# Optimization experiments

Hardware: AMD Instinct MI355X
Metric: run time of the kernel (lower is better)

## Reference

```python
import jax, jax.numpy as jnp
import numpy as np

MAX_LEVEL = 50

def _ln(x, g, b, eps=1e-5):
    m = jnp.mean(x, axis=-1, keepdims=True)
    v = jnp.mean((x - m) ** 2, axis=-1, keepdims=True)
    return (x - m) * jax.lax.rsqrt(v + eps) * g + b

def _mlp2(x, w1, b1, w2, b2):
    return jax.nn.relu(x @ w1 + b1) @ w2 + b2

def _forward(tokens, ln_g, ln_b, pw1, pb1, pw2, pb2, emb,
             sw1, sb1, sw2, sb2, ew1, eb1, ew2, eb2,
             spw1, spb1, spw2, spb2, lw1, lb1, lw2, lb2,
             fw, fb, fg, fbeta, aW, ab, ag, abt,
             dw1, db1, dw2, db2, levels, ph, pw):
    N = tokens.shape[0]
    f32 = tokens.dtype
    # token_norm + token_projection (Dropout is identity in eval)
    x = _ln(tokens, ln_g, ln_b)
    h = jax.nn.gelu(x @ pw1 + pb1, approximate=False) @ pw2 + pb2  # [N, D]
    idx = jnp.clip(levels[:, 0], 0, MAX_LEVEL)  # [N]
    h = h + emb[idx]
    # feature enhancement branch
    var = jnp.var(tokens, axis=-1, ddof=1, keepdims=True)            # torch.var unbiased
    mean = jnp.mean(tokens, axis=-1, keepdims=True)
    edge = jnp.mean(jnp.abs(jnp.diff(tokens, axis=-1)), axis=-1, keepdims=True)
    stats_feat = _mlp2(jnp.concatenate([var, mean], -1), sw1, sb1, sw2, sb2)
    spatial = jnp.broadcast_to(jnp.array([[ph, pw]], dtype=f32), (N, 2))
    spatial_feat = _mlp2(spatial, spw1, spb1, spw2, spb2)
    edge_feat = _mlp2(edge, ew1, eb1, ew2, eb2)
    lvl = jnp.broadcast_to(levels[0, 0].astype(f32)[None, None], (N, 1))
    level_feat = _mlp2(lvl, lw1, lb1, lw2, lb2)
    enh = jnp.concatenate([stats_feat, edge_feat, spatial_feat, level_feat], -1)  # [N, D]
    enh = jax.nn.gelu(_ln(enh @ fw + fb, fg, fbeta), approximate=False)
    h = h + 0.3 * enh
    # per-token scale adapter: MoE-style gather + tiny per-token GEMM + per-expert LN + GELU
    y = jnp.einsum('nd,ndf->nf', h, aW[idx]) + ab[idx]
    y = jax.nn.gelu(_ln(y, ag[idx], abt[idx]), approximate=False)
    # dynamic weighting gate
    w = jax.nn.sigmoid(_mlp2(y, dw1, db1, dw2, db2))  # [N, 1]
    return y * (0.8 + 0.4 * w)


def setup_inputs() -> dict:
    key = jax.random.key(0)
    ks = iter(jax.random.split(key, 64))
    def rn(shape, s=0.02):
        return jax.random.normal(next(ks), shape, dtype=jnp.float32) * s
    IN, D, D2, D4, DH, E, N = 768, 256, 512, 64, 128, 51, 4096
    return {
        'tokens': jax.random.normal(next(ks), (N, IN), dtype=jnp.float32),
        'ln_g': jnp.ones((IN,)), 'ln_b': jnp.zeros((IN,)),
        'pw1': rn((IN, D2)), 'pb1': jnp.zeros((D2,)),
        'pw2': rn((D2, D)), 'pb2': jnp.zeros((D,)),
        'emb': rn((E, D), 1.0),
        'sw1': rn((2, D4)), 'sb1': jnp.zeros((D4,)), 'sw2': rn((D4, D4)), 'sb2': jnp.zeros((D4,)),
        'ew1': rn((1, D4)), 'eb1': jnp.zeros((D4,)), 'ew2': rn((D4, D4)), 'eb2': jnp.zeros((D4,)),
        'spw1': rn((2, D4)), 'spb1': jnp.zeros((D4,)), 'spw2': rn((D4, D4)), 'spb2': jnp.zeros((D4,)),
        'lw1': rn((1, D4)), 'lb1': jnp.zeros((D4,)), 'lw2': rn((D4, D4)), 'lb2': jnp.zeros((D4,)),
        'fw': rn((D, D)), 'fb': jnp.zeros((D,)), 'fg': jnp.ones((D,)), 'fbeta': jnp.zeros((D,)),
        'aW': rn((E, D, D)), 'ab': jnp.zeros((E, D)), 'ag': jnp.ones((E, D)), 'abt': jnp.zeros((E, D)),
        'dw1': rn((D, DH)), 'db1': jnp.zeros((DH,)), 'dw2': rn((DH, 1)), 'db2': jnp.zeros((1,)),
        'levels': jax.random.randint(next(ks), (N, 2), 0, E),
        'ph': 4, 'pw': 4,
    }


def reference(tokens, ln_g, ln_b, pw1, pb1, pw2, pb2, emb,
              sw1, sb1, sw2, sb2, ew1, eb1, ew2, eb2,
              spw1, spb1, spw2, spb2, lw1, lb1, lw2, lb2,
              fw, fb, fg, fbeta, aW, ab, ag, abt,
              dw1, db1, dw2, db2, levels, ph, pw):
    return _forward(tokens, ln_g, ln_b, pw1, pb1, pw2, pb2, emb,
                    sw1, sb1, sw2, sb2, ew1, eb1, ew2, eb2,
                    spw1, spb1, spw2, spb2, lw1, lb1, lw2, lb2,
                    fw, fb, fg, fbeta, aW, ab, ag, abt,
                    dw1, db1, dw2, db2, levels, ph, pw)
```

## Files before the change

### kernel.cpp

```cpp
#include <hip/hip_runtime.h>
#include <math.h>

#define NTOK 4096
#define IND 768
#define DD 256
#define DD2 512
#define DHH 128
#define NEXP 51
#define TM 32
#define NTILE_MAX 179
#define NWCONV 968

typedef __attribute__((ext_vector_type(4))) float f32x4;
typedef __attribute__((ext_vector_type(8))) short short8;

__device__ __forceinline__ float gelu_f(float x) {
    return 0.5f * x * (1.0f + erff(x * 0.70710678118654752440f));
}
__device__ __forceinline__ ushort f2bf(float x) {
    unsigned u = __float_as_uint(x);
    return (ushort)((u + 0x7fffu + ((u >> 16) & 1u)) >> 16);
}
__device__ __forceinline__ void gl_lds16(const ushort* g, ushort* l) {
    __builtin_amdgcn_global_load_lds(
        (const __attribute__((address_space(1))) unsigned int*)g,
        (__attribute__((address_space(3))) unsigned int*)l, 16, 0, 0);
}

__global__ __launch_bounds__(256) void k_pre(
    const float* __restrict__ pw1, const float* __restrict__ pw2,
    const float* __restrict__ fw, const float* __restrict__ dw1,
    const float* __restrict__ aW,
    ushort* __restrict__ pw1T, ushort* __restrict__ pw2T, ushort* __restrict__ fwT,
    ushort* __restrict__ dw1T, ushort* __restrict__ aWT,
    const float* __restrict__ tokens,
    const float* __restrict__ ln_g, const float* __restrict__ ln_b,
    const float* __restrict__ sw1, const float* __restrict__ sb1,
    const float* __restrict__ sw2, const float* __restrict__ sb2,
    const float* __restrict__ ew1, const float* __restrict__ eb1,
    const float* __restrict__ ew2, const float* __restrict__ eb2,
    ushort* __restrict__ x_ln, ushort* __restrict__ enh,
    const int* __restrict__ levels,
    const float* __restrict__ spw1, const float* __restrict__ spb1,
    const float* __restrict__ spw2, const float* __restrict__ spb2,
    const float* __restrict__ lw1, const float* __restrict__ lb1,
    const float* __restrict__ lw2, const float* __restrict__ lb2,
    const int* __restrict__ ph, const int* __restrict__ pw,
    const float* __restrict__ fb,
    int* __restrict__ sorted, int* __restrict__ tpos, int* __restrict__ tcnt,
    int* __restrict__ texp, int* __restrict__ meta, float* __restrict__ ctail) {
    __shared__ float T[64][65];
    __shared__ int cnt[NEXP], cur[NEXP], offS[NEXP + 1], tileoff[NEXP + 1];
    __shared__ int expS[NTOK];
    __shared__ float hsS[64], hlS[64], cf[128];
    int t = threadIdx.x;

    if (blockIdx.x == 0) {
        if (t < NEXP) cnt[t] = 0;
        if (t < 64) {
            float p0 = (float)ph[0], p1 = (float)pw[0];
            float lvl = (float)levels[0];
            hsS[t] = fmaxf(0.f, p0 * spw1[t] + p1 * spw1[64 + t] + spb1[t]);
            hlS[t] = fmaxf(0.f, lvl * lw1[t] + lb1[t]);
        }
        __syncthreads();
        int myidx[16];
        #pragma unroll
        for (int i = 0; i < 16; ++i) {
            int n = t + i * 256;
            int id = min(max(levels[n * 2], 0), NEXP - 1);
            myidx[i] = id;
            atomicAdd(&cnt[id], 1);
        }
        if (t < 64) {
            float v = spb2[t];
            for (int j = 0; j < 64; ++j) v += hsS[j] * spw2[j * 64 + t];
            cf[t] = v;
        } else if (t < 128) {
            int k = t - 64;
            float v = lb2[k];
            for (int j = 0; j < 64; ++j) v += hlS[j] * lw2[j * 64 + k];
            cf[64 + k] = v;
        }
        __syncthreads();
        if (t == 0) {
            int a = 0, ta = 0;
            for (int e = 0; e < NEXP; ++e) {
                offS[e] = a; cur[e] = a; tileoff[e] = ta;
                ta += (cnt[e] + TM - 1) / TM;
                a += cnt[e];
            }
            offS[NEXP] = a; tileoff[NEXP] = ta;
            meta[0] = ta;
        }
        __syncthreads();
        #pragma unroll
        for (int i = 0; i < 16; ++i) {
            int n = t + i * 256;
            int p = atomicAdd(&cur[myidx[i]], 1);
            sorted[p] = n;
            expS[p] = myidx[i];
        }
        {
            float v = fb[t];
            for (int j = 0; j < 128; ++j) v += cf[j] * fw[(size_t)(128 + j) * DD + t];
            ctail[t] = v;
        }
        __syncthreads();
        #pragma unroll
        for (int i = 0; i < 16; ++i) {
            int p = t + i * 256;
            int e = expS[p];
            int rel = p - offS[e];
            if ((rel & (TM - 1)) == 0) {
                int ti = tileoff[e] + (rel / TM);
                tpos[ti] = p;
                tcnt[ti] = min(TM, offS[e + 1] - p);
                texp[ti] = e;
            }
        }
        return;
    }
    if (blockIdx.x < 1 + NWCONV) {
        int b = blockIdx.x - 1;
        const float* src; ushort* dst; int R, C;
        if (b < 96)       { src = pw1; dst = pw1T; R = IND; C = DD2; }
        else if (b < 128) { b -= 96;  src = pw2; dst = pw2T; R = DD2; C = DD; }
        else if (b < 144) { b -= 128; src = fw;  dst = fwT;  R = DD;  C = DD; }
        else if (b < 152) { b -= 144; src = dw1; dst = dw1T; R = DD;  C = DHH; }
        else { b -= 152; int e = b >> 4; b &= 15;
               src = aW + (size_t)e * DD * DD; dst = aWT + (size_t)e * DD * DD;
               R = DD; C = DD; }
        int tpc = C >> 6;
        int tr = b / tpc, tc = b - tr * tpc;
        int lr = t >> 6, lc = t & 63;
        #pragma unroll
        for (int i = 0; i < 16; ++i) {
            int r = i * 4 + lr;
            T[r][lc] = src[(size_t)(tr * 64 + r) * C + tc * 64 + lc];
        }
        __syncthreads();
        #pragma unroll
        for (int i = 0; i < 16; ++i) {
            int r = i * 4 + lr;
            dst[(size_t)(tc * 64 + r) * R + tr * 64 + lc] = f2bf(T[lc][r]);
        }
        return;
    }
    {
        int w = t >> 6, lane = t & 63;
        int n = (blockIdx.x - 1 - NWCONV) * 4 + w;
        const float* x = tokens + (size_t)n * IND;
        float v[12];
        {
            float4 va = *(const float4*)(x + lane * 12);
            float4 vb = *(const float4*)(x + lane * 12 + 4);
            float4 vc = *(const float4*)(x + lane * 12 + 8);
            v[0]=va.x; v[1]=va.y; v[2]=va.z; v[3]=va.w;
            v[4]=vb.x; v[5]=vb.y; v[6]=vb.z; v[7]=vb.w;
            v[8]=vc.x; v[9]=vc.y; v[10]=vc.z; v[11]=vc.w;
        }
        float s = 0.f, s2 = 0.f, es = 0.f;
        #pragma unroll
        for (int j = 0; j < 12; ++j) { s += v[j]; s2 += v[j] * v[j]; }
        float prev = __shfl_up(v[11], 1);
        if (lane > 0) es += fabsf(v[0] - prev);
        #pragma unroll
        for (int j = 1; j < 12; ++j) es += fabsf(v[j] - v[j - 1]);
        #pragma unroll
        for (int o = 1; o < 64; o <<= 1) {
            s  += __shfl_xor(s, o);
            s2 += __shfl_xor(s2, o);
            es += __shfl_xor(es, o);
        }
        float mean = s * (1.f / 768.f);
        float var_u = (s2 - 768.f * mean * mean) * (1.f / 767.f);
        float rstd = rsqrtf(s2 * (1.f / 768.f) - mean * mean + 1e-5f);
        float edge = es * (1.f / 767.f);
        ushort xl[12];
        #pragma unroll
        for (int j = 0; j < 12; ++j) {
            int e = lane * 12 + j;
            xl[j] = f2bf((v[j] - mean) * rstd * ln_g[e] + ln_b[e]);
        }
        ushort* xd = x_ln + (size_t)n * IND + lane * 12;
        *(ushort4*)(xd)     = *(ushort4*)&xl[0];
        *(ushort4*)(xd + 4) = *(ushort4*)&xl[4];
        *(ushort4*)(xd + 8) = *(ushort4*)&xl[8];
        float hs_ = fmaxf(0.f, var_u * sw1[lane] + mean * sw1[64 + lane] + sb1[lane]);
        float he_ = fmaxf(0.f, edge * ew1[lane] + eb1[lane]);
        float acc_s = sb2[lane], acc_e = eb2[lane];
        #pragma unroll 8
        for (int j = 0; j < 64; ++j) {
            float hj = __shfl(hs_, j);
            float ej = __shfl(he_, j);
            acc_s += hj * sw2[j * 64 + lane];
            acc_e += ej * ew2[j * 64 + lane];
        }
        ushort* er = enh + (size_t)n * DHH;
        er[lane] = f2bf(acc_s);
        er[64 + lane] = f2bf(acc_e);
    }
}

__global__ __launch_bounds__(512) void k_gemm1(
    const ushort* __restrict__ A, const ushort* __restrict__ BT,
    const float* __restrict__ bias, ushort* __restrict__ Cb) {
    const int N = DD2, K = IND;
    __shared__ ushort Al[128][64];
    __shared__ ushort Bl[64][64];
    int tid = threadIdx.x;
    int w = tid >> 6, lane = tid & 63;
    int g = lane >> 4, mr = lane & 15;
    int mq = w >> 1, nq = w & 1;
    int bm = blockIdx.y * 128, bn = blockIdx.x * 64;
    int r8 = lane >> 3, c = lane & 7, cg = c ^ r8;
    f32x4 acc[2][2];
    #pragma unroll
    for (int im = 0; im < 2; ++im)
        #pragma unroll
        for (int in = 0; in < 2; ++in) acc[im][in] = (f32x4){0.f, 0.f, 0.f, 0.f};
    for (int k0 = 0; k0 < K; k0 += 64) {
        #pragma unroll
        for (int i = 0; i < 2; ++i) {
            int r = 16 * w + 8 * i + r8;
            gl_lds16(A + (size_t)(bm + r) * K + k0 + cg * 8, &Al[16 * w + 8 * i][0]);
        }
        {
            int r = 8 * w + r8;
            gl_lds16(BT + (size_t)(bn + r) * K + k0 + cg * 8, &Bl[8 * w][0]);
        }
        asm volatile("s_waitcnt vmcnt(0)" ::: "memory");
        __syncthreads();
        #pragma unroll
        for (int kk = 0; kk < 64; kk += 32) {
            int jc = (kk >> 3) + g;
            int sw = ((jc ^ (mr & 7)) << 4);
            #pragma unroll
            for (int im = 0; im < 2; ++im) {
                short8 av = *(const short8*)((const char*)&Al[0][0] + (32 * mq + 16 * im + mr) * 128 + sw);
                #pragma unroll
                for (int in = 0; in < 2; ++in) {
                    short8 bv = *(const short8*)((const char*)&Bl[0][0] + (32 * nq + 16 * in + mr) * 128 + sw);
                    acc[im][in] = __builtin_amdgcn_mfma_f32_16x16x32_bf16(av, bv, acc[im][in], 0, 0, 0);
                }
            }
        }
        __syncthreads();
    }
    #pragma unroll
    for (int im = 0; im < 2; ++im) {
        #pragma unroll
        for (int in = 0; in < 2; ++in) {
            int col = bn + 32 * nq + 16 * in + mr;
            float bv = bias[col];
            #pragma unroll
            for (int r = 0; r < 4; ++r) {
                int row = bm + 32 * mq + 16 * im + 4 * g + r;
                Cb[(size_t)row * N + col] = f2bf(gelu_f(acc[im][in][r] + bv));
            }
        }
    }
}

__global__ __launch_bounds__(512) void k_adapterF(
    const ushort* __restrict__ h1, const ushort* __restrict__ enh,
    const ushort* __restrict__ pw2T, const float* __restrict__ pb2,
    const float* __restrict__ emb,
    const ushort* __restrict__ fwT, const float* __restrict__ ctail,
    const float* __restrict__ fg, const float* __restrict__ fbeta,
    const ushort* __restrict__ aWT, const float* __restrict__ ab,
    const float* __restrict__ ag, const float* __restrict__ abt,
    const ushort* __restrict__ dw1T, const float* __restrict__ db1,
    const float* __restrict__ dw2, const float* __restrict__ db2,
    const int* __restrict__ sorted, const int* __restrict__ tpos,
    const int* __restrict__ tcnt, const int* __restrict__ texp,
    const int* __restrict__ meta, float* __restrict__ out) {
    __shared__ __align__(16) char smA[33280];
    __shared__ __align__(16) char smB[33280];
    __shared__ __align__(16) ushort EnhS[TM][128];
    __shared__ int tokS[TM];
    __shared__ float redS[4][TM][2];
    __shared__ float gateS[TM];
    __shared__ float pg[4][TM];
    ushort* H1p = (ushort*)smA;
    ushort* Alf = (ushort*)smA;
    ushort* Dlp = (ushort*)(smA + 16896);
    ushort* Blp = (ushort*)smB;
    float* yf32 = (float*)smB;

    int b = blockIdx.x;
    if (b >= meta[0]) return;
    int tid = threadIdx.x, w = tid >> 6, lane = tid & 63;
    int g = lane >> 4, mr = lane & 15;
    int r8 = lane >> 3, c = lane & 7, cg = c ^ r8;
    int mt = w & 1, cb = 64 * (w >> 1);
    int e = texp[b], base = tpos[b], nv = tcnt[b];
    if (tid < TM) tokS[tid] = sorted[base + min(tid, nv - 1)];
    __syncthreads();

    #pragma unroll
    for (int i = 0; i < 4; ++i) {
        int r = 4 * w + i;
        int tok = tokS[r];
        gl_lds16(h1 + (size_t)tok * DD2 + ((lane ^ (r & 7)) << 3), H1p + r * DD2);
    }
    {
        int row = 4 * w + (lane >> 4);
        int tok = tokS[row];
        int ch = lane & 15;
        gl_lds16(enh + (size_t)tok * DHH + ((ch ^ (row & 7)) << 3), &EnhS[4 * w][0]);
    }
    asm volatile("s_waitcnt vmcnt(0)" ::: "memory");
    __syncthreads();

    f32x4 hacc[4];
    #pragma unroll
    for (int q = 0; q < 4; ++q) hacc[q] = (f32x4){0.f, 0.f, 0.f, 0.f};
    for (int k0 = 0; k0 < DD2; k0 += 64) {
        #pragma unroll
        for (int i = 0; i < 4; ++i) {
            int r = 32 * w + 8 * i + r8;
            gl_lds16(pw2T + (size_t)r * DD2 + k0 + cg * 8, Blp + (32 * w + 8 * i) * 64);
        }
        asm volatile("s_waitcnt vmcnt(0)" ::: "memory");
        __syncthreads();
        #pragma unroll
        for (int kk = 0; kk < 64; kk += 32) {
            int jc = ((k0 + kk) >> 3) + g;
            short8 av = *(const short8*)((const char*)H1p + (16 * mt + mr) * 1024 + ((jc ^ (mr & 7)) << 4));
            int swb = (((kk >> 3) + g) ^ (mr & 7)) << 4;
            #pragma unroll
            for (int q = 0; q < 4; ++q) {
                short8 bv = *(const short8*)((const char*)Blp + (cb + 16 * q + mr) * 128 + swb);
                hacc[q] = __builtin_amdgcn_mfma_f32_16x16x32_bf16(av, bv, hacc[q], 0, 0, 0);
            }
        }
        __syncthreads();
    }
    f32x4 eacc[4];
    #pragma unroll
    for (int q = 0; q < 4; ++q) eacc[q] = (f32x4){0.f, 0.f, 0.f, 0.f};
    for (int k0 = 0; k0 < DHH; k0 += 64) {
        #pragma unroll
        for (int i = 0; i < 4; ++i) {
            int r = 32 * w + 8 * i + r8;
            gl_lds16(fwT + (size_t)r * DD + k0 + cg * 8, Blp + (32 * w + 8 * i) * 64);
        }
        asm volatile("s_waitcnt vmcnt(0)" ::: "memory");
        __syncthreads();
        #pragma unroll
        for (int kk = 0; kk < 64; kk += 32) {
            int jc = ((k0 + kk) >> 3) + g;
            short8 av = *(const short8*)((const char*)&EnhS[0][0] + (16 * mt + mr) * 256 + ((jc ^ (mr & 7)) << 4));
            int swb = (((kk >> 3) + g) ^ (mr & 7)) << 4;
            #pragma unroll
            for (int q = 0; q < 4; ++q) {
                short8 bv = *(const short8*)((const char*)Blp + (cb + 16 * q + mr) * 128 + swb);
                eacc[q] = __builtin_amdgcn_mfma_f32_16x16x32_bf16(av, bv, eacc[q], 0, 0, 0);
            }
        }
        __syncthreads();
    }
    #pragma unroll
    for (int q = 0; q < 4; ++q) {
        int col = cb + 16 * q + mr;
        float hb = pb2[col] + emb[(size_t)e * DD + col];
        float cb2 = ctail[col];
        #pragma unroll
        for (int r4 = 0; r4 < 4; ++r4) {
            hacc[q][r4] += hb;
            eacc[q][r4] += cb2;
        }
    }
    {
        float s[4], s2[4];
        #pragma unroll
        for (int r4 = 0; r4 < 4; ++r4) {
            s[r4] = eacc[0][r4] + eacc[1][r4] + eacc[2][r4] + eacc[3][r4];
            s2[r4] = eacc[0][r4]*eacc[0][r4] + eacc[1][r4]*eacc[1][r4]
                   + eacc[2][r4]*eacc[2][r4] + eacc[3][r4]*eacc[3][r4];
        }
        #pragma unroll
        for (int o = 1; o < 16; o <<= 1) {
            #pragma unroll
            for (int r4 = 0; r4 < 4; ++r4) {
                s[r4]  += __shfl_xor(s[r4], o);
                s2[r4] += __shfl_xor(s2[r4], o);
            }
        }
        if (mr == 0) {
            #pragma unroll
            for (int r4 = 0; r4 < 4; ++r4) {
                int row = 16 * mt + 4 * g + r4;
                redS[w >> 1][row][0] = s[r4];
                redS[w >> 1][row][1] = s2[r4];
            }
        }
    }
    __syncthreads();
    #pragma unroll
    for (int r4 = 0; r4 < 4; ++r4) {
        int row = 16 * mt + 4 * g + r4;
        float S  = redS[0][row][0] + redS[1][row][0] + redS[2][row][0] + redS[3][row][0];
        float S2 = redS[0][row][1] + redS[1][row][1] + redS[2][row][1] + redS[3][row][1];
        float m = S * (1.f / 256.f);
        float rs = rsqrtf(S2 * (1.f / 256.f) - m * m + 1e-5f);
        #pragma unroll
        for (int q = 0; q < 4; ++q) {
            int col = cb + 16 * q + mr;
            float enhv = gelu_f((eacc[q][r4] - m) * rs * fg[col] + fbeta[col]);
            Alf[row * 264 + col] = f2bf(hacc[q][r4] + 0.3f * enhv);
        }
    }
    __syncthreads();
    const ushort* We = aWT + (size_t)e * DD * DD;
    f32x4 yacc[4];
    #pragma unroll
    for (int q = 0; q < 4; ++q) yacc[q] = (f32x4){0.f, 0.f, 0.f, 0.f};
    for (int k0 = 0; k0 < DD; k0 += 64) {
        #pragma unroll
        for (int i = 0; i < 4; ++i) {
            int r = 32 * w + 8 * i + r8;
            gl_lds16(We + (size_t)r * DD + k0 + cg * 8, Blp + (32 * w + 8 * i) * 64);
        }
        asm volatile("s_waitcnt vmcnt(0)" ::: "memory");
        __syncthreads();
        #pragma unroll
        for (int kk = 0; kk < 64; kk += 32) {
            short8 av = *(const short8*)&Alf[(16 * mt + mr) * 264 + k0 + kk + g * 8];
            int swb = (((kk >> 3) + g) ^ (mr & 7)) << 4;
            #pragma unroll
            for (int q = 0; q < 4; ++q) {
                short8 bv = *(const short8*)((const char*)Blp + (cb + 16 * q + mr) * 128 + swb);
                yacc[q] = __builtin_amdgcn_mfma_f32_16x16x32_bf16(av, bv, yacc[q], 0, 0, 0);
            }
        }
        __syncthreads();
    }
    #pragma unroll
    for (int q = 0; q < 4; ++q) {
        int col = cb + 16 * q + mr;
        float abv = ab[(size_t)e * DD + col];
        #pragma unroll
        for (int r4 = 0; r4 < 4; ++r4) {
            int row = 16 * mt + 4 * g + r4;
            yf32[row * 260 + col] = yacc[q][r4] + abv;
        }
    }
    __syncthreads();
    #pragma unroll
    for (int i = 0; i < 4; ++i) {
        int r = 4 * w + i;
        float4 v = *(const float4*)&yf32[r * 260 + lane * 4];
        float s = v.x + v.y + v.z + v.w;
        float s2 = v.x * v.x + v.y * v.y + v.z * v.z + v.w * v.w;
        #pragma unroll
        for (int o = 1; o < 64; o <<= 1) { s += __shfl_xor(s, o); s2 += __shfl_xor(s2, o); }
        float m = s * (1.f / 256.f);
        float rs = rsqrtf(s2 * (1.f / 256.f) - m * m + 1e-5f);
        float4 gg = *(const float4*)(ag + (size_t)e * DD + lane * 4);
        float4 bb = *(const float4*)(abt + (size_t)e * DD + lane * 4);
        float4 y;
        y.x = gelu_f((v.x - m) * rs * gg.x + bb.x);
        y.y = gelu_f((v.y - m) * rs * gg.y + bb.y);
        y.z = gelu_f((v.z - m) * rs * gg.z + bb.z);
        y.w = gelu_f((v.w - m) * rs * gg.w + bb.w);
        *(float4*)&yf32[r * 260 + lane * 4] = y;
        ushort4 o4 = {f2bf(y.x), f2bf(y.y), f2bf(y.z), f2bf(y.w)};
        *(ushort4*)&Alf[r * 264 + lane * 4] = o4;
    }
    __syncthreads();
    f32x4 acc2[2];
    acc2[0] = (f32x4){0.f, 0.f, 0.f, 0.f};
    acc2[1] = (f32x4){0.f, 0.f, 0.f, 0.f};
    for (int k0 = 0; k0 < DD; k0 += 64) {
        #pragma unroll
        for (int i = 0; i < 2; ++i) {
            int r = 16 * w + 8 * i + r8;
            gl_lds16(dw1T + (size_t)r * DD + k0 + cg * 8, Dlp + (16 * w + 8 * i) * 64);
        }
        asm volatile("s_waitcnt vmcnt(0)" ::: "memory");
        __syncthreads();
        #pragma unroll
        for (int kk = 0; kk < 64; kk += 32) {
            short8 av = *(const short8*)&Alf[(16 * mt + mr) * 264 + k0 + kk + g * 8];
            int swb = (((kk >> 3) + g) ^ (mr & 7)) << 4;
            #pragma unroll
            for (int q = 0; q < 2; ++q) {
                short8 bv = *(const short8*)((const char*)Dlp + (32 * (w >> 1) + 16 * q + mr) * 128 + swb);
                acc2[q] = __builtin_amdgcn_mfma_f32_16x16x32_bf16(av, bv, acc2[q], 0, 0, 0);
            }
        }
        __syncthreads();
    }
    float pv[4] = {0.f, 0.f, 0.f, 0.f};
    #pragma unroll
    for (int q = 0; q < 2; ++q) {
        int col = 32 * (w >> 1) + 16 * q + mr;
        float d1 = db1[col], d2 = dw2[col];
        #pragma unroll
        for (int r4 = 0; r4 < 4; ++r4)
            pv[r4] += fmaxf(acc2[q][r4] + d1, 0.f) * d2;
    }
    #pragma unroll
    for (int o = 1; o < 16; o <<= 1) {
        #pragma unroll
        for (int r4 = 0; r4 < 4; ++r4) pv[r4] += __shfl_xor(pv[r4], o);
    }
    if (mr == 0) {
        #pragma unroll
        for (int r4 = 0; r4 < 4; ++r4)
            pg[w >> 1][16 * mt + 4 * g + r4] = pv[r4];
    }
    __syncthreads();
    if (tid < TM) {
        float p = pg[0][tid] + pg[1][tid] + pg[2][tid] + pg[3][tid] + db2[0];
        gateS[tid] = 0.8f + 0.4f / (1.f + expf(-p));
    }
    __syncthreads();
    {
        int row = tid >> 4, c0 = (tid & 15) * 16;
        if (row < nv) {
            int tok = tokS[row];
            float gt = gateS[row];
            #pragma unroll
            for (int j = 0; j < 4; ++j) {
                float4 v = *(const float4*)&yf32[row * 260 + c0 + j * 4];
                v.x *= gt; v.y *= gt; v.z *= gt; v.w *= gt;
                *(float4*)(out + (size_t)tok * DD + c0 + j * 4) = v;
            }
        }
    }
}

extern "C" void kernel_launch(void* const* d_in, const int* in_sizes, int n_in,
                              void* d_out, int out_size, void* d_ws, size_t ws_size,
                              hipStream_t stream) {
    const float* tokens = (const float*)d_in[0];
    const float* ln_g = (const float*)d_in[1];
    const float* ln_b = (const float*)d_in[2];
    const float* pw1 = (const float*)d_in[3];
    const float* pb1 = (const float*)d_in[4];
    const float* pw2 = (const float*)d_in[5];
    const float* pb2 = (const float*)d_in[6];
    const float* emb = (const float*)d_in[7];
    const float* sw1 = (const float*)d_in[8];
    const float* sb1 = (const float*)d_in[9];
    const float* sw2 = (const float*)d_in[10];
    const float* sb2 = (const float*)d_in[11];
    const float* ew1 = (const float*)d_in[12];
    const float* eb1 = (const float*)d_in[13];
    const float* ew2 = (const float*)d_in[14];
    const float* eb2 = (const float*)d_in[15];
    const float* spw1 = (const float*)d_in[16];
    const float* spb1 = (const float*)d_in[17];
    const float* spw2 = (const float*)d_in[18];
    const float* spb2 = (const float*)d_in[19];
    const float* lw1 = (const float*)d_in[20];
    const float* lb1 = (const float*)d_in[21];
    const float* lw2 = (const float*)d_in[22];
    const float* lb2 = (const float*)d_in[23];
    const float* fw = (const float*)d_in[24];
    const float* fb = (const float*)d_in[25];
    const float* fg = (const float*)d_in[26];
    const float* fbeta = (const float*)d_in[27];
    const float* aW = (const float*)d_in[28];
    const float* ab = (const float*)d_in[29];
    const float* ag = (const float*)d_in[30];
    const float* abt = (const float*)d_in[31];
    const float* dw1 = (const float*)d_in[32];
    const float* db1 = (const float*)d_in[33];
    const float* dw2 = (const float*)d_in[34];
    const float* db2 = (const float*)d_in[35];
    const int* levels = (const int*)d_in[36];
    const int* ph = (const int*)d_in[37];
    const int* pw = (const int*)d_in[38];
    float* outp = (float*)d_out;

    char* wsb = (char*)d_ws;
    ushort* x_ln  = (ushort*)wsb;  wsb += (size_t)NTOK * IND * 2;
    ushort* h1    = (ushort*)wsb;  wsb += (size_t)NTOK * DD2 * 2;
    ushort* enh   = (ushort*)wsb;  wsb += (size_t)NTOK * DHH * 2;
    ushort* pw1T  = (ushort*)wsb;  wsb += (size_t)DD2 * IND * 2;
    ushort* pw2T  = (ushort*)wsb;  wsb += (size_t)DD * DD2 * 2;
    ushort* fwT   = (ushort*)wsb;  wsb += (size_t)DD * DD * 2;
    ushort* aWT   = (ushort*)wsb;  wsb += (size_t)NEXP * DD * DD * 2;
    ushort* dw1T  = (ushort*)wsb;  wsb += (size_t)DHH * DD * 2;
    float*  ctail = (float*)wsb;   wsb += DD * 4;
    int*    sorted = (int*)wsb;    wsb += NTOK * 4;
    int*    tpos   = (int*)wsb;    wsb += NTILE_MAX * 4;
    int*    tcnt   = (int*)wsb;    wsb += NTILE_MAX * 4;
    int*    texp   = (int*)wsb;    wsb += NTILE_MAX * 4;
    int*    meta   = (int*)wsb;    wsb += 64;

    k_pre<<<1 + NWCONV + NTOK / 4, 256, 0, stream>>>(
        pw1, pw2, fw, dw1, aW, pw1T, pw2T, fwT, dw1T, aWT,
        tokens, ln_g, ln_b, sw1, sb1, sw2, sb2, ew1, eb1, ew2, eb2,
        x_ln, enh, levels,
        spw1, spb1, spw2, spb2, lw1, lb1, lw2, lb2, ph, pw, fb,
        sorted, tpos, tcnt, texp, meta, ctail);
    k_gemm1<<<dim3(DD2 / 64, NTOK / 128), 512, 0, stream>>>(x_ln, pw1T, pb1, h1);
    k_adapterF<<<NTILE_MAX, 512, 0, stream>>>(
        h1, enh, pw2T, pb2, emb, fwT, ctail, fg, fbeta,
        aWT, ab, ag, abt, dw1T, db1, dw2, db2,
        sorted, tpos, tcnt, texp, meta, outp);
}
```

Before: 65.50 us.

## Halve adapter token tile to 16 rows and remap warps to column slices

Shrinks the per-expert token tile from 32 to 16 rows, so each of the 8 warps now owns a 32-column slice of all 16 rows instead of a 16x64 block. More, smaller tiles reduce padding waste in per-expert groups and cut shared memory per block, which can raise occupancy and block count. In the prep kernel the expert-index buffer is aliased onto the transpose scratch to save LDS. The cost is that each expert's weight matrix is reloaded by more blocks, and cross-warp reductions now span 8 partial sums.

```diff
diff --git a/kernel.cpp b/kernel.cpp
--- a/kernel.cpp
+++ b/kernel.cpp
@@ -7,8 +7,8 @@
 #define DD2 512
 #define DHH 128
 #define NEXP 51
-#define TM 32
-#define NTILE_MAX 179
+#define TM 16
+#define NTILE_MAX 312
 #define NWCONV 968
 
 typedef __attribute__((ext_vector_type(4))) float f32x4;
@@ -49,9 +49,10 @@
     const float* __restrict__ fb,
     int* __restrict__ sorted, int* __restrict__ tpos, int* __restrict__ tcnt,
     int* __restrict__ texp, int* __restrict__ meta, float* __restrict__ ctail) {
-    __shared__ float T[64][65];
+    __shared__ __align__(16) char TU[16640];
+    float (*T)[65] = (float(*)[65])TU;
+    int* expS = (int*)TU;
     __shared__ int cnt[NEXP], cur[NEXP], offS[NEXP + 1], tileoff[NEXP + 1];
-    __shared__ int expS[NTOK];
     __shared__ float hsS[64], hlS[64], cf[128];
     int t = threadIdx.x;
 
@@ -276,16 +277,16 @@
     const int* __restrict__ sorted, const int* __restrict__ tpos,
     const int* __restrict__ tcnt, const int* __restrict__ texp,
     const int* __restrict__ meta, float* __restrict__ out) {
-    __shared__ __align__(16) char smA[33280];
-    __shared__ __align__(16) char smB[33280];
+    __shared__ __align__(16) char smA[24832];
+    __shared__ __align__(16) char smB[32768];
     __shared__ __align__(16) ushort EnhS[TM][128];
     __shared__ int tokS[TM];
-    __shared__ float redS[4][TM][2];
+    __shared__ float redS[8][TM][2];
     __shared__ float gateS[TM];
-    __shared__ float pg[4][TM];
+    __shared__ float pg[8][TM];
     ushort* H1p = (ushort*)smA;
     ushort* Alf = (ushort*)smA;
-    ushort* Dlp = (ushort*)(smA + 16896);
+    ushort* Dlp = (ushort*)(smA + 8448);
     ushort* Blp = (ushort*)smB;
     float* yf32 = (float*)smB;
 
@@ -294,18 +295,18 @@
     int tid = threadIdx.x, w = tid >> 6, lane = tid & 63;
     int g = lane >> 4, mr = lane & 15;
     int r8 = lane >> 3, c = lane & 7, cg = c ^ r8;
-    int mt = w & 1, cb = 64 * (w >> 1);
+    int cb = 32 * w;
     int e = texp[b], base = tpos[b], nv = tcnt[b];
     if (tid < TM) tokS[tid] = sorted[base + min(tid, nv - 1)];
     __syncthreads();
 
     #pragma unroll
-    for (int i = 0; i < 4; ++i) {
-        int r = 4 * w + i;
+    for (int i = 0; i < 2; ++i) {
+        int r = 2 * w + i;
         int tok = tokS[r];
         gl_lds16(h1 + (size_t)tok * DD2 + ((lane ^ (r & 7)) << 3), H1p + r * DD2);
     }
-    {
+    if (w < 4) {
         int row = 4 * w + (lane >> 4);
         int tok = tokS[row];
         int ch = lane & 15;
@@ -314,9 +315,9 @@
     asm volatile("s_waitcnt vmcnt(0)" ::: "memory");
     __syncthreads();
 
-    f32x4 hacc[4];
-    #pragma unroll
-    for (int q = 0; q < 4; ++q) hacc[q] = (f32x4){0.f, 0.f, 0.f, 0.f};
+    f32x4 hacc[2];
+    hacc[0] = (f32x4){0.f, 0.f, 0.f, 0.f};
+    hacc[1] = (f32x4){0.f, 0.f, 0.f, 0.f};
     for (int k0 = 0; k0 < DD2; k0 += 64) {
         #pragma unroll
         for (int i = 0; i < 4; ++i) {
@@ -328,19 +329,19 @@
         #pragma unroll
         for (int kk = 0; kk < 64; kk += 32) {
             int jc = ((k0 + kk) >> 3) + g;
-            short8 av = *(const short8*)((const char*)H1p + (16 * mt + mr) * 1024 + ((jc ^ (mr & 7)) << 4));
+            short8 av = *(const short8*)((const char*)H1p + mr * 1024 + ((jc ^ (mr & 7)) << 4));
             int swb = (((kk >> 3) + g) ^ (mr & 7)) << 4;
             #pragma unroll
-            for (int q = 0; q < 4; ++q) {
+            for (int q = 0; q < 2; ++q) {
                 short8 bv = *(const short8*)((const char*)Blp + (cb + 16 * q + mr) * 128 + swb);
                 hacc[q] = __builtin_amdgcn_mfma_f32_16x16x32_bf16(av, bv, hacc[q], 0, 0, 0);
             }
         }
         __syncthreads();
     }
-    f32x4 eacc[4];
-    #pragma unroll
-    for (int q = 0; q < 4; ++q) eacc[q] = (f32x4){0.f, 0.f, 0.f, 0.f};
+    f32x4 eacc[2];
+    eacc[0] = (f32x4){0.f, 0.f, 0.f, 0.f};
+    eacc[1] = (f32x4){0.f, 0.f, 0.f, 0.f};
     for (int k0 = 0; k0 < DHH; k0 += 64) {
         #pragma unroll
         for (int i = 0; i < 4; ++i) {
@@ -352,10 +353,10 @@
         #pragma unroll
         for (int kk = 0; kk < 64; kk += 32) {
             int jc = ((k0 + kk) >> 3) + g;
-            short8 av = *(const short8*)((const char*)&EnhS[0][0] + (16 * mt + mr) * 256 + ((jc ^ (mr & 7)) << 4));
+            short8 av = *(const short8*)((const char*)&EnhS[0][0] + mr * 256 + ((jc ^ (mr & 7)) << 4));
             int swb = (((kk >> 3) + g) ^ (mr & 7)) << 4;
             #pragma unroll
-            for (int q = 0; q < 4; ++q) {
+            for (int q = 0; q < 2; ++q) {
                 short8 bv = *(const short8*)((const char*)Blp + (cb + 16 * q + mr) * 128 + swb);
                 eacc[q] = __builtin_amdgcn_mfma_f32_16x16x32_bf16(av, bv, eacc[q], 0, 0, 0);
             }
@@ -363,7 +364,7 @@
         __syncthreads();
     }
     #pragma unroll
-    for (int q = 0; q < 4; ++q) {
+    for (int q = 0; q < 2; ++q) {
         int col = cb + 16 * q + mr;
         float hb = pb2[col] + emb[(size_t)e * DD + col];
         float cb2 = ctail[col];
@@ -377,9 +378,8 @@
         float s[4], s2[4];
         #pragma unroll
         for (int r4 = 0; r4 < 4; ++r4) {
-            s[r4] = eacc[0][r4] + eacc[1][r4] + eacc[2][r4] + eacc[3][r4];
-            s2[r4] = eacc[0][r4]*eacc[0][r4] + eacc[1][r4]*eacc[1][r4]
-                   + eacc[2][r4]*eacc[2][r4] + eacc[3][r4]*eacc[3][r4];
+            s[r4] = eacc[0][r4] + eacc[1][r4];
+            s2[r4] = eacc[0][r4] * eacc[0][r4] + eacc[1][r4] * eacc[1][r4];
         }
         #pragma unroll
         for (int o = 1; o < 16; o <<= 1) {
@@ -392,22 +392,22 @@
         if (mr == 0) {
             #pragma unroll
             for (int r4 = 0; r4 < 4; ++r4) {
-                int row = 16 * mt + 4 * g + r4;
-                redS[w >> 1][row][0] = s[r4];
-                redS[w >> 1][row][1] = s2[r4];
+                redS[w][4 * g + r4][0] = s[r4];
+                redS[w][4 * g + r4][1] = s2[r4];
             }
         }
     }
     __syncthreads();
     #pragma unroll
     for (int r4 = 0; r4 < 4; ++r4) {
-        int row = 16 * mt + 4 * g + r4;
-        float S  = redS[0][row][0] + redS[1][row][0] + redS[2][row][0] + redS[3][row][0];
-        float S2 = redS[0][row][1] + redS[1][row][1] + redS[2][row][1] + redS[3][row][1];
+        int row = 4 * g + r4;
+        float S = 0.f, S2 = 0.f;
+        #pragma unroll
+        for (int ww = 0; ww < 8; ++ww) { S += redS[ww][row][0]; S2 += redS[ww][row][1]; }
         float m = S * (1.f / 256.f);
         float rs = rsqrtf(S2 * (1.f / 256.f) - m * m + 1e-5f);
         #pragma unroll
-        for (int q = 0; q < 4; ++q) {
+        for (int q = 0; q < 2; ++q) {
             int col = cb + 16 * q + mr;
             float enhv = gelu_f((eacc[q][r4] - m) * rs * fg[col] + fbeta[col]);
             Alf[row * 264 + col] = f2bf(hacc[q][r4] + 0.3f * enhv);
@@ -415,9 +415,9 @@
     }
     __syncthreads();
     const ushort* We = aWT + (size_t)e * DD * DD;
-    f32x4 yacc[4];
-    #pragma unroll
-    for (int q = 0; q < 4; ++q) yacc[q] = (f32x4){0.f, 0.f, 0.f, 0.f};
+    f32x4 yacc[2];
+    yacc[0] = (f32x4){0.f, 0.f, 0.f, 0.f};
+    yacc[1] = (f32x4){0.f, 0.f, 0.f, 0.f};
     for (int k0 = 0; k0 < DD; k0 += 64) {
         #pragma unroll
         for (int i = 0; i < 4; ++i) {
@@ -428,10 +428,10 @@
         __syncthreads();
         #pragma unroll
         for (int kk = 0; kk < 64; kk += 32) {
-            short8 av = *(const short8*)&Alf[(16 * mt + mr) * 264 + k0 + kk + g * 8];
+            short8 av = *(const short8*)&Alf[mr * 264 + k0 + kk + g * 8];
             int swb = (((kk >> 3) + g) ^ (mr & 7)) << 4;
             #pragma unroll
-            for (int q = 0; q < 4; ++q) {
+            for (int q = 0; q < 2; ++q) {
                 short8 bv = *(const short8*)((const char*)Blp + (cb + 16 * q + mr) * 128 + swb);
                 yacc[q] = __builtin_amdgcn_mfma_f32_16x16x32_bf16(av, bv, yacc[q], 0, 0, 0);
             }
@@ -439,19 +439,18 @@
         __syncthreads();
     }
     #pragma unroll
-    for (int q = 0; q < 4; ++q) {
+    for (int q = 0; q < 2; ++q) {
         int col = cb + 16 * q + mr;
         float abv = ab[(size_t)e * DD + col];
         #pragma unroll
         for (int r4 = 0; r4 < 4; ++r4) {
-            int row = 16 * mt + 4 * g + r4;
-            yf32[row * 260 + col] = yacc[q][r4] + abv;
+            yf32[(4 * g + r4) * 260 + col] = yacc[q][r4] + abv;
         }
     }
     __syncthreads();
     #pragma unroll
-    for (int i = 0; i < 4; ++i) {
-        int r = 4 * w + i;
+    for (int i = 0; i < 2; ++i) {
+        int r = 2 * w + i;
         float4 v = *(const float4*)&yf32[r * 260 + lane * 4];
         float s = v.x + v.y + v.z + v.w;
         float s2 = v.x * v.x + v.y * v.y + v.z * v.z + v.w * v.w;
@@ -471,9 +470,7 @@
         *(ushort4*)&Alf[r * 264 + lane * 4] = o4;
     }
     __syncthreads();
-    f32x4 acc2[2];
-    acc2[0] = (f32x4){0.f, 0.f, 0.f, 0.f};
-    acc2[1] = (f32x4){0.f, 0.f, 0.f, 0.f};
+    f32x4 acc2 = (f32x4){0.f, 0.f, 0.f, 0.f};
     for (int k0 = 0; k0 < DD; k0 += 64) {
         #pragma unroll
         for (int i = 0; i < 2; ++i) {
@@ -484,48 +481,46 @@
         __syncthreads();
         #pragma unroll
         for (int kk = 0; kk < 64; kk += 32) {
-            short8 av = *(const short8*)&Alf[(16 * mt + mr) * 264 + k0 + kk + g * 8];
+            short8 av = *(const short8*)&Alf[mr * 264 + k0 + kk + g * 8];
             int swb = (((kk >> 3) + g) ^ (mr & 7)) << 4;
-            #pragma unroll
-            for (int q = 0; q < 2; ++q) {
-                short8 bv = *(const short8*)((const char*)Dlp + (32 * (w >> 1) + 16 * q + mr) * 128 + swb);
-                acc2[q] = __builtin_amdgcn_mfma_f32_16x16x32_bf16(av, bv, acc2[q], 0, 0, 0);
-            }
-        }
-        __syncthreads();
-    }
-    float pv[4] = {0.f, 0.f, 0.f, 0.f};
-    #pragma unroll
-    for (int q = 0; q < 2; ++q) {
-        int col = 32 * (w >> 1) + 16 * q + mr;
+            short8 bv = *(const short8*)((const char*)Dlp + (16 * w + mr) * 128 + swb);
+            acc2 = __builtin_amdgcn_mfma_f32_16x16x32_bf16(av, bv, acc2, 0, 0, 0);
+        }
+        __syncthreads();
+    }
+    {
+        int col = 16 * w + mr;
         float d1 = db1[col], d2 = dw2[col];
+        float pv[4];
         #pragma unroll
         for (int r4 = 0; r4 < 4; ++r4)
-            pv[r4] += fmaxf(acc2[q][r4] + d1, 0.f) * d2;
-    }
-    #pragma unroll
-    for (int o = 1; o < 16; o <<= 1) {
-        #pragma unroll
-        for (int r4 = 0; r4 < 4; ++r4) pv[r4] += __shfl_xor(pv[r4], o);
-    }
-    if (mr == 0) {
-        #pragma unroll
-        for (int r4 = 0; r4 < 4; ++r4)
-            pg[w >> 1][16 * mt + 4 * g + r4] = pv[r4];
+            pv[r4] = fmaxf(acc2[r4] + d1, 0.f) * d2;
+        #pragma unroll
+        for (int o = 1; o < 16; o <<= 1) {
+            #pragma unroll
+            for (int r4 = 0; r4 < 4; ++r4) pv[r4] += __shfl_xor(pv[r4], o);
+        }
+        if (mr == 0) {
+            #pragma unroll
+            for (int r4 = 0; r4 < 4; ++r4)
+                pg[w][4 * g + r4] = pv[r4];
+        }
     }
     __syncthreads();
     if (tid < TM) {
-        float p = pg[0][tid] + pg[1][tid] + pg[2][tid] + pg[3][tid] + db2[0];
+        float p = db2[0];
+        #pragma unroll
+        for (int ww = 0; ww < 8; ++ww) p += pg[ww][tid];
         gateS[tid] = 0.8f + 0.4f / (1.f + expf(-p));
     }
     __syncthreads();
     {
-        int row = tid >> 4, c0 = (tid & 15) * 16;
+        int row = tid >> 5, c0 = (tid & 31) * 8;
         if (row < nv) {
             int tok = tokS[row];
             float gt = gateS[row];
             #pragma unroll
-            for (int j = 0; j < 4; ++j) {
+            for (int j = 0; j < 2; ++j) {
                 float4 v = *(const float4*)&yf32[row * 260 + c0 + j * 4];
                 v.x *= gt; v.y *= gt; v.z *= gt; v.w *= gt;
                 *(float4*)(out + (size_t)tok * DD + c0 + j * 4) = v;
```

Result: faster. 63.47 us (-3.1%).
